# Kernel tuning notes

Hardware: AMD Instinct MI355X
Metric: run time of the kernel (lower is better)

## Reference

```python
import jax, jax.numpy as jnp
import numpy as np

HEAD_DIM = 64
NUM_HEADS = 16
ROPE_BASE = 10000.0


def _rope_cos_sin(seq_len, head_dim, dtype):
    inv_freq = 1.0 / (ROPE_BASE ** (jnp.arange(0, head_dim, 2, dtype=jnp.float32) / head_dim))
    t = jnp.arange(seq_len, dtype=jnp.float32)
    freqs = jnp.outer(t, inv_freq)                      # [S, D/2]
    emb = jnp.concatenate([freqs, freqs], axis=-1)      # [S, D]
    return jnp.cos(emb).astype(dtype), jnp.sin(emb).astype(dtype)


def _rotate_half(x):
    x1, x2 = jnp.split(x, 2, axis=-1)
    return jnp.concatenate([-x2, x1], axis=-1)


def setup_inputs() -> dict:
    key = jax.random.key(0)
    ks = jax.random.split(key, 5)
    B, S, H = 2, 2048, 1024
    x = jax.random.normal(ks[0], (B, S, H), dtype=jnp.float32)
    attention_mask = jnp.ones((B, S), dtype=jnp.float32)
    scale = 0.02
    Wq = jax.random.normal(ks[1], (H, H), dtype=jnp.float32) * scale
    Wk = jax.random.normal(ks[2], (H, H), dtype=jnp.float32) * scale
    Wv = jax.random.normal(ks[3], (H, H), dtype=jnp.float32) * scale
    Wo = jax.random.normal(ks[4], (H, H), dtype=jnp.float32) * scale
    return {"x": x, "attention_mask": attention_mask, "Wq": Wq, "Wk": Wk, "Wv": Wv, "Wo": Wo}


def reference(x, attention_mask, Wq, Wk, Wv, Wo):
    B, S, H = x.shape
    nh, hd = NUM_HEADS, HEAD_DIM
    scale = hd ** -0.5

    # nn.Linear semantics: y = x @ W^T  (W is [out, in])
    q = jnp.einsum('bsh,oh->bso', x, Wq).reshape(B, S, nh, hd).transpose(0, 2, 1, 3)
    k = jnp.einsum('bsh,oh->bso', x, Wk).reshape(B, S, nh, hd).transpose(0, 2, 1, 3)
    v = jnp.einsum('bsh,oh->bso', x, Wv).reshape(B, S, nh, hd).transpose(0, 2, 1, 3)

    cos, sin = _rope_cos_sin(S, hd, x.dtype)            # [S, hd]
    cos = cos[None, None, :, :]
    sin = sin[None, None, :, :]
    q = q * cos + _rotate_half(q) * sin
    k = k * cos + _rotate_half(k) * sin

    attn = jnp.einsum('bhqd,bhkd->bhqk', q, k) * scale  # [B, nh, S, S]
    mask = (1.0 - attention_mask.astype(x.dtype))[:, None, None, :] * jnp.finfo(x.dtype).min
    attn = attn + mask
    attn = jax.nn.softmax(attn, axis=-1)
    out = jnp.einsum('bhqk,bhkd->bhqd', attn, v)        # [B, nh, S, hd]
    out = out.transpose(0, 2, 1, 3).reshape(B, S, nh * hd)
    return jnp.einsum('bso,ho->bsh', out, Wo)
```

## Files before the change

### kernel.cpp

```cpp
#include <hip/hip_runtime.h>
#include <math.h>

#define BB 2
#define SS 2048
#define HH 1024
#define NH 16
#define HD 64
#define MM (BB*SS)

typedef __attribute__((ext_vector_type(8))) _Float16 f16x8;
typedef __attribute__((ext_vector_type(2))) __fp16 hf16x2;
typedef __attribute__((ext_vector_type(4))) float f32x4;
typedef __attribute__((ext_vector_type(16))) float f32x16;

#define QSCALE 0.18033688011112042f

__device__ __forceinline__ unsigned short f2h(float f) {
    union { _Float16 h; unsigned short u; } c;
    c.h = (_Float16)f;
    return c.u;
}

__device__ __forceinline__ unsigned int pkh(float a, float b) {
    union { hf16x2 h; unsigned int u; } c;
    c.h = __builtin_amdgcn_cvt_pkrtz(a, b);
    return c.u;
}

__device__ __forceinline__ void gld16(const void* g, void* s) {
    __builtin_amdgcn_global_load_lds(
        (const __attribute__((address_space(1))) void*)g,
        (__attribute__((address_space(3))) void*)s, 16, 0, 0);
}

__global__ __launch_bounds__(256) void prep(
    const float* __restrict__ x, const float* __restrict__ mask,
    const float* __restrict__ Wq, const float* __restrict__ Wk,
    const float* __restrict__ Wv, const float* __restrict__ Wo,
    unsigned short* __restrict__ xf, unsigned short* __restrict__ wf,
    float* __restrict__ ctab, float* __restrict__ stab, float* __restrict__ mt,
    unsigned int* __restrict__ mflag)
{
    int gtid = blockIdx.x * 256 + threadIdx.x;
    if (gtid < SS * 32) {
        int s = gtid >> 5, i = gtid & 31;
        double invf = pow(10000.0, -(double)i / 32.0);
        double a = (double)s * invf;
        ctab[gtid] = (float)cos(a);
        stab[gtid] = (float)sin(a);
    }
    if (gtid < BB * SS) {
        float mv = mask[gtid];
        mt[gtid] = (1.0f - mv) * (-1.0e38f);
        unsigned long long bal = __ballot(mv == 1.0f);
        if ((threadIdx.x & 63) == 0)
            mflag[gtid >> 6] = (bal == ~0ull) ? 1u : 0u;
    }
    for (int it = gtid; it < 2097152; it += 524288) {
        float4 v; unsigned short* d; size_t off;
        if (it < 1048576) {
            off = (size_t)it * 4;
            v = *(const float4*)(x + off);
            d = xf;
        } else {
            off = (size_t)(it - 1048576) * 4;
            int row = (int)(off >> 10);
            const float* W = row < 1024 ? Wq : row < 2048 ? Wk : row < 3072 ? Wv : Wo;
            v = *(const float4*)(W + (((size_t)(row & 1023)) << 10) + (off & 1023));
            d = wf;
        }
        *(ushort4*)(d + off) = make_ushort4(f2h(v.x), f2h(v.y), f2h(v.z), f2h(v.w));
    }
}

template<int MODE>
__global__ __launch_bounds__(256, 3) void gemm3(
    const unsigned short* __restrict__ Axf,
    const unsigned short* __restrict__ Wf,
    const float* __restrict__ ctab, const float* __restrict__ stab,
    unsigned short* __restrict__ qo, unsigned short* __restrict__ ko,
    unsigned short* __restrict__ vo, float* __restrict__ fout)
{
    __shared__ __align__(16) short lsA[2][128*32];
    __shared__ __align__(16) short lsB[2][128*32];

    const int t = threadIdx.x;
    const int m0 = blockIdx.x * 128;
    const int brow0 = (MODE == 0 ? 0 : 3072) + blockIdx.y * 128;
    const int lane = t & 63, wv = t >> 6;
    const int wm = (wv >> 1) * 64, wn = (wv & 1) * 64;
    const int fr = lane & 15, fg = lane >> 4;

    const int srow = t >> 2, pc = t & 3;
    const int scx = (pc ^ ((srow >> 1) & 3)) * 8;
    const int lo  = srow * 32 + pc * 8;
    const size_t gA0 = (size_t)(m0 + srow) * HH + scx;
    const size_t gA1 = (size_t)(m0 + 64 + srow) * HH + scx;
    const size_t gB0 = (size_t)(brow0 + srow) * HH + scx;
    const size_t gB1 = (size_t)(brow0 + 64 + srow) * HH + scx;

    f32x4 acc[4][4] = {};

#define STAGE(sel, kk) do { \
        gld16(Axf + gA0 + (kk), &lsA[sel][lo]);            \
        gld16(Wf  + gB0 + (kk), &lsB[sel][lo]);            \
        gld16(Axf + gA1 + (kk), &lsA[sel][lo + 64*32]);    \
        gld16(Wf  + gB1 + (kk), &lsB[sel][lo + 64*32]);    \
    } while (0)

    STAGE(0, 0);
    __syncthreads();

    int cur = 0;
    for (int k0 = 0; k0 < HH; k0 += 32) {
        if (k0 + 32 < HH) STAGE(cur ^ 1, k0 + 32);

        f16x8 ah[4], bh[4];
        const int swz = (fg ^ ((fr >> 1) & 3)) * 8;
        #pragma unroll
        for (int mi = 0; mi < 4; ++mi)
            ah[mi] = *(const f16x8*)&lsA[cur][(wm + 16*mi + fr)*32 + swz];
        #pragma unroll
        for (int ni = 0; ni < 4; ++ni)
            bh[ni] = *(const f16x8*)&lsB[cur][(wn + 16*ni + fr)*32 + swz];

        __builtin_amdgcn_s_setprio(1);
        #pragma unroll
        for (int mi = 0; mi < 4; ++mi)
            #pragma unroll
            for (int ni = 0; ni < 4; ++ni)
                acc[mi][ni] = __builtin_amdgcn_mfma_f32_16x16x32_f16(ah[mi], bh[ni], acc[mi][ni], 0, 0, 0);
        __builtin_amdgcn_s_setprio(0);
        __syncthreads();
        cur ^= 1;
    }
#undef STAGE

    if (MODE == 0) {
        const int mat = brow0 >> 10;
        const int obase = (brow0 & 1023) + wn;
        const int h = obase >> 6;
        #pragma unroll
        for (int mi = 0; mi < 4; ++mi)
            #pragma unroll
            for (int rr = 0; rr < 4; ++rr) {
                int m = m0 + wm + 16*mi + 4*fg + rr;
                int b = m >> 11, s = m & (SS - 1);
                float v[4];
                #pragma unroll
                for (int ni = 0; ni < 4; ++ni) v[ni] = acc[mi][ni][rr];
                if (mat < 2) {
                    #pragma unroll
                    for (int ni = 0; ni < 2; ++ni) {
                        int i = 16*ni + fr;
                        float c = ctab[s*32 + i], sn = stab[s*32 + i];
                        float v1 = v[ni], v2 = v[ni + 2];
                        v[ni]     = v1*c - v2*sn;
                        v[ni + 2] = v2*c + v1*sn;
                    }
                }
                if (mat == 0) {
                    #pragma unroll
                    for (int ni = 0; ni < 4; ++ni) v[ni] *= QSCALE;
                }
                size_t base = ((size_t)(b*NH + h) * SS + s) * HD;
                #pragma unroll
                for (int ni = 0; ni < 4; ++ni) {
                    int d = 16*ni + fr;
                    unsigned short hb = f2h(v[ni]);
                    if (mat == 0)      qo[base + d] = hb;
                    else if (mat == 1) ko[base + (d ^ ((s & 7) << 3))] = hb;
                    else {
                        size_t va = ((size_t)(b*NH + h) * HD + d) * SS
                                  + (s & ~63) + ((s & 63) ^ ((d & 7) << 3));
                        vo[va] = hb;
                    }
                }
            }
    } else {
        const int n0 = blockIdx.y * 128 + wn;
        #pragma unroll
        for (int mi = 0; mi < 4; ++mi)
            #pragma unroll
            for (int rr = 0; rr < 4; ++rr) {
                int m = m0 + wm + 16*mi + 4*fg + rr;
                #pragma unroll
                for (int ni = 0; ni < 4; ++ni)
                    fout[(size_t)m * HH + n0 + 16*ni + fr] = acc[mi][ni][rr];
            }
    }
}

__global__ __launch_bounds__(256, 4) void attn(
    const unsigned short* __restrict__ qg, const unsigned short* __restrict__ kg,
    const unsigned short* __restrict__ vtg, const float* __restrict__ mt,
    const unsigned int* __restrict__ mfl, unsigned short* __restrict__ cf)
{
    __shared__ __align__(16) short Ks[2][64*64];
    __shared__ __align__(16) short Vs[2][64*64];

    const int t = threadIdx.x, lane = t & 63, wv = t >> 6;
    const int ql = lane & 31;
    const int u  = lane >> 5;
    const int qx = ql & 7;
    const int qh = wv & 1, kh = wv >> 1;
    const int flat = blockIdx.x;
    const int bh = (flat & 7) + ((flat >> 8) << 3);
    const int q0 = ((flat >> 3) & 31) * 64;
    const int b = bh >> 4, h = bh & 15;

    const unsigned short* kgb = kg  + (size_t)bh*SS*HD;
    const unsigned short* vgb = vtg + (size_t)bh*HD*SS;
    const float* mtb = mt + (size_t)b*SS;
    const unsigned int* mfb = mfl + b*32;

    f16x8 qa[4];
    #pragma unroll
    for (int dc = 0; dc < 4; ++dc)
        qa[dc] = *(const f16x8*)&qg[((size_t)bh*SS + q0 + 32*qh + ql)*HD + 16*dc + 8*u];

    f32x16 o[2] = {};
    float lpart = 0.f;

    const int srow = t >> 3, sg = t & 7;

    gld16(kgb + (size_t)srow*HD + sg*8,      &Ks[0][srow*64 + sg*8]);
    gld16(kgb + (size_t)(32+srow)*HD + sg*8, &Ks[0][(32+srow)*64 + sg*8]);
    gld16(vgb + (size_t)srow*SS + sg*8,      &Vs[0][srow*64 + sg*8]);
    gld16(vgb + (size_t)(32+srow)*SS + sg*8, &Vs[0][(32+srow)*64 + sg*8]);
    __syncthreads();

    int cur = 0;
    for (int kt = 0; kt < SS/64; ++kt) {
        const int k0 = kt * 64;
        if (kt + 1 < SS/64) {
            const int kn = k0 + 64;
            gld16(kgb + (size_t)(kn+srow)*HD + sg*8,      &Ks[cur^1][srow*64 + sg*8]);
            gld16(kgb + (size_t)(kn+32+srow)*HD + sg*8,   &Ks[cur^1][(32+srow)*64 + sg*8]);
            gld16(vgb + (size_t)srow*SS + kn + sg*8,      &Vs[cur^1][srow*64 + sg*8]);
            gld16(vgb + (size_t)(32+srow)*SS + kn + sg*8, &Vs[cur^1][(32+srow)*64 + sg*8]);
        }
        const int fl = __builtin_amdgcn_readfirstlane(mfb[kt]);

        f16x8 kb[4];
        #pragma unroll
        for (int dc = 0; dc < 4; ++dc)
            kb[dc] = *(const f16x8*)&Ks[cur][(32*kh + ql)*64 + ((2*dc + u) ^ qx)*8];

        f32x16 sc = {};
        __builtin_amdgcn_s_setprio(1);
        #pragma unroll
        for (int dc = 0; dc < 4; ++dc)
            sc = __builtin_amdgcn_mfma_f32_32x32x16_f16(kb[dc], qa[dc], sc, 0, 0, 0);
        __builtin_amdgcn_s_setprio(0);

        f16x8 vb[2][2];
        #pragma unroll
        for (int dt = 0; dt < 2; ++dt)
            #pragma unroll
            for (int ki = 0; ki < 2; ++ki)
                vb[dt][ki] = *(const f16x8*)&Vs[cur][(32*dt + ql)*64 + ((4*kh + 2*ki + u) ^ qx)*8];

        if (fl) {
            #pragma unroll
            for (int r = 0; r < 16; ++r) {
                float p = __builtin_amdgcn_exp2f(sc[r]);
                sc[r] = p;
                lpart += p;
            }
        } else {
            #pragma unroll
            for (int g = 0; g < 4; ++g) {
                float4 m4 = *(const float4*)&mtb[k0 + 32*kh + 8*g + 4*u];
                #pragma unroll
                for (int j = 0; j < 4; ++j) {
                    float p = __builtin_amdgcn_exp2f(sc[4*g + j] + (&m4.x)[j]);
                    sc[4*g + j] = p;
                    lpart += p;
                }
            }
        }

        __builtin_amdgcn_s_setprio(1);
        #pragma unroll
        for (int ki = 0; ki < 2; ++ki) {
            const int R0 = 8 * ki;
            unsigned int A0 = pkh(sc[R0+0], sc[R0+1]);
            unsigned int A1 = pkh(sc[R0+2], sc[R0+3]);
            unsigned int B0 = pkh(sc[R0+4], sc[R0+5]);
            unsigned int B1 = pkh(sc[R0+6], sc[R0+7]);
            asm volatile("v_permlane32_swap_b32 %0, %1" : "+v"(A0), "+v"(B0));
            asm volatile("v_permlane32_swap_b32 %0, %1" : "+v"(A1), "+v"(B1));
            union { unsigned int w[4]; f16x8 v; } pf;
            pf.w[0] = A0; pf.w[1] = A1; pf.w[2] = B0; pf.w[3] = B1;
            #pragma unroll
            for (int dt = 0; dt < 2; ++dt)
                o[dt] = __builtin_amdgcn_mfma_f32_32x32x16_f16(vb[dt][ki], pf.v, o[dt], 0, 0, 0);
        }
        __builtin_amdgcn_s_setprio(0);
        __syncthreads();
        cur ^= 1;
    }

    float* lscr = (float*)Vs;
    float* oscr = (float*)Ks;
    if (kh == 1) lscr[qh*64 + lane] = lpart;
    __syncthreads();
    float inv = 0.f;
    if (kh == 0) {
        float l = lpart + lscr[qh*64 + lane];
        l += __shfl_xor(l, 32);
        inv = 1.0f / l;
    }
    const size_t base = ((size_t)b*SS + q0 + 32*qh + ql)*HH + h*HD;
    #pragma unroll
    for (int dt = 0; dt < 2; ++dt) {
        __syncthreads();
        if (kh == 1) {
            #pragma unroll
            for (int r = 0; r < 16; ++r)
                oscr[r*128 + qh*64 + lane] = o[dt][r];
        }
        __syncthreads();
        if (kh == 0) {
            #pragma unroll
            for (int g = 0; g < 4; ++g) {
                float v0 = (o[dt][4*g+0] + oscr[(4*g+0)*128 + qh*64 + lane]) * inv;
                float v1 = (o[dt][4*g+1] + oscr[(4*g+1)*128 + qh*64 + lane]) * inv;
                float v2 = (o[dt][4*g+2] + oscr[(4*g+2)*128 + qh*64 + lane]) * inv;
                float v3 = (o[dt][4*g+3] + oscr[(4*g+3)*128 + qh*64 + lane]) * inv;
                uint2 w; w.x = pkh(v0, v1); w.y = pkh(v2, v3);
                *(uint2*)&cf[base + 32*dt + 8*g + 4*u] = w;
            }
        }
    }
}

extern "C" void kernel_launch(void* const* d_in, const int* in_sizes, int n_in,
                              void* d_out, int out_size, void* d_ws, size_t ws_size,
                              hipStream_t stream) {
    const float* x    = (const float*)d_in[0];
    const float* mask = (const float*)d_in[1];
    const float* Wq   = (const float*)d_in[2];
    const float* Wk   = (const float*)d_in[3];
    const float* Wv   = (const float*)d_in[4];
    const float* Wo   = (const float*)d_in[5];
    float* out = (float*)d_out;

    const size_t T = (size_t)MM * HH;
    unsigned short* xf = (unsigned short*)d_ws;
    unsigned short* wf = xf + T;
    unsigned short* qt = wf + T;
    unsigned short* kt = qt + T;
    unsigned short* vt = kt + T;
    float* ctab = (float*)(vt + T);
    float* stab = ctab + SS*32;
    float* mt   = stab + SS*32;
    unsigned int* mfg = (unsigned int*)(mt + BB*SS);
    unsigned short* cf = xf;

    prep<<<2048, 256, 0, stream>>>(x, mask, Wq, Wk, Wv, Wo, xf, wf, ctab, stab, mt, mfg);
    gemm3<0><<<dim3(MM/128, 3*HH/128), 256, 0, stream>>>(xf, wf, ctab, stab,
                                                         qt, kt, vt, nullptr);
    attn<<<1024, 256, 0, stream>>>(qt, kt, vt, mt, mfg, cf);
    gemm3<1><<<dim3(MM/128, HH/128), 256, 0, stream>>>(cf, wf, nullptr, nullptr,
                                                       nullptr, nullptr, nullptr, out);
}
```

Baseline: 117.1 us.

## Load K/V fragments straight from global into registers, bypassing shared memory

The attention kernel no longer stages K and V tiles through double-buffered LDS with barriers. Each wave now loads its MFMA operand fragments directly from global memory into registers, using a two-set software pipeline. The QKV projection epilogue drops the XOR swizzle that existed for LDS bank-conflict avoidance, and launch bounds drop to 3 blocks per SIMD to make room for the extra registers. This removes the LDS traffic and per-tile syncthreads, but each wave now reads K/V itself, which duplicates global/L2 reads across the waves that share a tile and uses more registers.

New measurement: 186.4 us. 59.2% more time.

```diff
diff --git a/kernel.cpp b/kernel.cpp
--- a/kernel.cpp
+++ b/kernel.cpp
@@ -169,12 +169,8 @@
                     int d = 16*ni + fr;
                     unsigned short hb = f2h(v[ni]);
                     if (mat == 0)      qo[base + d] = hb;
-                    else if (mat == 1) ko[base + (d ^ ((s & 7) << 3))] = hb;
-                    else {
-                        size_t va = ((size_t)(b*NH + h) * HD + d) * SS
-                                  + (s & ~63) + ((s & 63) ^ ((d & 7) << 3));
-                        vo[va] = hb;
-                    }
+                    else if (mat == 1) ko[base + d] = hb;
+                    else vo[((size_t)(b*NH + h) * HD + d) * SS + s] = hb;
                 }
             }
     } else {
@@ -191,28 +187,27 @@
     }
 }
 
-__global__ __launch_bounds__(256, 4) void attn(
+__global__ __launch_bounds__(256, 3) void attn(
     const unsigned short* __restrict__ qg, const unsigned short* __restrict__ kg,
     const unsigned short* __restrict__ vtg, const float* __restrict__ mt,
     const unsigned int* __restrict__ mfl, unsigned short* __restrict__ cf)
 {
-    __shared__ __align__(16) short Ks[2][64*64];
-    __shared__ __align__(16) short Vs[2][64*64];
+    __shared__ float scr[2048 + 128];
 
     const int t = threadIdx.x, lane = t & 63, wv = t >> 6;
     const int ql = lane & 31;
     const int u  = lane >> 5;
-    const int qx = ql & 7;
     const int qh = wv & 1, kh = wv >> 1;
     const int flat = blockIdx.x;
     const int bh = (flat & 7) + ((flat >> 8) << 3);
     const int q0 = ((flat >> 3) & 31) * 64;
     const int b = bh >> 4, h = bh & 15;
 
-    const unsigned short* kgb = kg  + (size_t)bh*SS*HD;
-    const unsigned short* vgb = vtg + (size_t)bh*HD*SS;
     const float* mtb = mt + (size_t)b*SS;
     const unsigned int* mfb = mfl + b*32;
+
+    const unsigned short* kp = kg  + ((size_t)bh*SS + 32*kh + ql)*HD + 8*u;
+    const unsigned short* vp = vtg + ((size_t)bh*HD + ql)*SS + 32*kh + 8*u;
 
     f16x8 qa[4];
     #pragma unroll
@@ -222,88 +217,82 @@
     f32x16 o[2] = {};
     float lpart = 0.f;
 
-    const int srow = t >> 3, sg = t & 7;
-
-    gld16(kgb + (size_t)srow*HD + sg*8,      &Ks[0][srow*64 + sg*8]);
-    gld16(kgb + (size_t)(32+srow)*HD + sg*8, &Ks[0][(32+srow)*64 + sg*8]);
-    gld16(vgb + (size_t)srow*SS + sg*8,      &Vs[0][srow*64 + sg*8]);
-    gld16(vgb + (size_t)(32+srow)*SS + sg*8, &Vs[0][(32+srow)*64 + sg*8]);
-    __syncthreads();
-
-    int cur = 0;
-    for (int kt = 0; kt < SS/64; ++kt) {
-        const int k0 = kt * 64;
-        if (kt + 1 < SS/64) {
-            const int kn = k0 + 64;
-            gld16(kgb + (size_t)(kn+srow)*HD + sg*8,      &Ks[cur^1][srow*64 + sg*8]);
-            gld16(kgb + (size_t)(kn+32+srow)*HD + sg*8,   &Ks[cur^1][(32+srow)*64 + sg*8]);
-            gld16(vgb + (size_t)srow*SS + kn + sg*8,      &Vs[cur^1][srow*64 + sg*8]);
-            gld16(vgb + (size_t)(32+srow)*SS + kn + sg*8, &Vs[cur^1][(32+srow)*64 + sg*8]);
-        }
-        const int fl = __builtin_amdgcn_readfirstlane(mfb[kt]);
-
-        f16x8 kb[4];
-        #pragma unroll
-        for (int dc = 0; dc < 4; ++dc)
-            kb[dc] = *(const f16x8*)&Ks[cur][(32*kh + ql)*64 + ((2*dc + u) ^ qx)*8];
-
-        f32x16 sc = {};
-        __builtin_amdgcn_s_setprio(1);
-        #pragma unroll
-        for (int dc = 0; dc < 4; ++dc)
-            sc = __builtin_amdgcn_mfma_f32_32x32x16_f16(kb[dc], qa[dc], sc, 0, 0, 0);
-        __builtin_amdgcn_s_setprio(0);
-
-        f16x8 vb[2][2];
-        #pragma unroll
-        for (int dt = 0; dt < 2; ++dt)
-            #pragma unroll
-            for (int ki = 0; ki < 2; ++ki)
-                vb[dt][ki] = *(const f16x8*)&Vs[cur][(32*dt + ql)*64 + ((4*kh + 2*ki + u) ^ qx)*8];
-
-        if (fl) {
-            #pragma unroll
-            for (int r = 0; r < 16; ++r) {
-                float p = __builtin_amdgcn_exp2f(sc[r]);
-                sc[r] = p;
-                lpart += p;
-            }
-        } else {
-            #pragma unroll
-            for (int g = 0; g < 4; ++g) {
-                float4 m4 = *(const float4*)&mtb[k0 + 32*kh + 8*g + 4*u];
-                #pragma unroll
-                for (int j = 0; j < 4; ++j) {
-                    float p = __builtin_amdgcn_exp2f(sc[4*g + j] + (&m4.x)[j]);
-                    sc[4*g + j] = p;
-                    lpart += p;
-                }
-            }
-        }
-
-        __builtin_amdgcn_s_setprio(1);
-        #pragma unroll
-        for (int ki = 0; ki < 2; ++ki) {
-            const int R0 = 8 * ki;
-            unsigned int A0 = pkh(sc[R0+0], sc[R0+1]);
-            unsigned int A1 = pkh(sc[R0+2], sc[R0+3]);
-            unsigned int B0 = pkh(sc[R0+4], sc[R0+5]);
-            unsigned int B1 = pkh(sc[R0+6], sc[R0+7]);
-            asm volatile("v_permlane32_swap_b32 %0, %1" : "+v"(A0), "+v"(B0));
-            asm volatile("v_permlane32_swap_b32 %0, %1" : "+v"(A1), "+v"(B1));
-            union { unsigned int w[4]; f16x8 v; } pf;
-            pf.w[0] = A0; pf.w[1] = A1; pf.w[2] = B0; pf.w[3] = B1;
-            #pragma unroll
-            for (int dt = 0; dt < 2; ++dt)
-                o[dt] = __builtin_amdgcn_mfma_f32_32x32x16_f16(vb[dt][ki], pf.v, o[dt], 0, 0, 0);
-        }
-        __builtin_amdgcn_s_setprio(0);
-        __syncthreads();
-        cur ^= 1;
-    }
-
-    float* lscr = (float*)Vs;
-    float* oscr = (float*)Ks;
+    f16x8 Akb0, Akb1, Akb2, Akb3, Avb00, Avb01, Avb10, Avb11;
+    f16x8 Bkb0, Bkb1, Bkb2, Bkb3, Bvb00, Bvb01, Bvb10, Bvb11;
+
+#define LOADSET(P, kk) do {                                                   \
+        P##kb0  = *(const f16x8*)(kp + (size_t)(kk)*HD +  0);                 \
+        P##kb1  = *(const f16x8*)(kp + (size_t)(kk)*HD + 16);                 \
+        P##kb2  = *(const f16x8*)(kp + (size_t)(kk)*HD + 32);                 \
+        P##kb3  = *(const f16x8*)(kp + (size_t)(kk)*HD + 48);                 \
+        P##vb00 = *(const f16x8*)(vp + (kk) +  0);                            \
+        P##vb01 = *(const f16x8*)(vp + (kk) + 16);                            \
+        P##vb10 = *(const f16x8*)(vp + (size_t)32*SS + (kk) +  0);            \
+        P##vb11 = *(const f16x8*)(vp + (size_t)32*SS + (kk) + 16);            \
+    } while (0)
+
+#define COMPUTE(P, kk) do {                                                   \
+        const int fl = __builtin_amdgcn_readfirstlane(mfb[(kk) >> 6]);        \
+        f32x16 sc = {};                                                       \
+        __builtin_amdgcn_s_setprio(1);                                        \
+        sc = __builtin_amdgcn_mfma_f32_32x32x16_f16(P##kb0, qa[0], sc, 0, 0, 0); \
+        sc = __builtin_amdgcn_mfma_f32_32x32x16_f16(P##kb1, qa[1], sc, 0, 0, 0); \
+        sc = __builtin_amdgcn_mfma_f32_32x32x16_f16(P##kb2, qa[2], sc, 0, 0, 0); \
+        sc = __builtin_amdgcn_mfma_f32_32x32x16_f16(P##kb3, qa[3], sc, 0, 0, 0); \
+        __builtin_amdgcn_s_setprio(0);                                        \
+        if (fl) {                                                             \
+            _Pragma("unroll")                                                 \
+            for (int r = 0; r < 16; ++r) {                                    \
+                float p = __builtin_amdgcn_exp2f(sc[r]);                      \
+                sc[r] = p; lpart += p;                                        \
+            }                                                                 \
+        } else {                                                              \
+            _Pragma("unroll")                                                 \
+            for (int g = 0; g < 4; ++g) {                                     \
+                float4 m4 = *(const float4*)&mtb[(kk) + 32*kh + 8*g + 4*u];   \
+                _Pragma("unroll")                                             \
+                for (int j = 0; j < 4; ++j) {                                 \
+                    float p = __builtin_amdgcn_exp2f(sc[4*g + j] + (&m4.x)[j]); \
+                    sc[4*g + j] = p; lpart += p;                              \
+                }                                                             \
+            }                                                                 \
+        }                                                                     \
+        __builtin_amdgcn_s_setprio(1);                                        \
+        {                                                                     \
+            unsigned int A0 = pkh(sc[0], sc[1]), A1 = pkh(sc[2], sc[3]);      \
+            unsigned int B0 = pkh(sc[4], sc[5]), B1 = pkh(sc[6], sc[7]);      \
+            asm volatile("v_permlane32_swap_b32 %0, %1" : "+v"(A0), "+v"(B0));\
+            asm volatile("v_permlane32_swap_b32 %0, %1" : "+v"(A1), "+v"(B1));\
+            union { unsigned int w[4]; f16x8 v; } pf;                         \
+            pf.w[0] = A0; pf.w[1] = A1; pf.w[2] = B0; pf.w[3] = B1;           \
+            o[0] = __builtin_amdgcn_mfma_f32_32x32x16_f16(P##vb00, pf.v, o[0], 0, 0, 0); \
+            o[1] = __builtin_amdgcn_mfma_f32_32x32x16_f16(P##vb10, pf.v, o[1], 0, 0, 0); \
+        }                                                                     \
+        {                                                                     \
+            unsigned int A0 = pkh(sc[8], sc[9]),  A1 = pkh(sc[10], sc[11]);   \
+            unsigned int B0 = pkh(sc[12], sc[13]), B1 = pkh(sc[14], sc[15]);  \
+            asm volatile("v_permlane32_swap_b32 %0, %1" : "+v"(A0), "+v"(B0));\
+            asm volatile("v_permlane32_swap_b32 %0, %1" : "+v"(A1), "+v"(B1));\
+            union { unsigned int w[4]; f16x8 v; } pf;                         \
+            pf.w[0] = A0; pf.w[1] = A1; pf.w[2] = B0; pf.w[3] = B1;           \
+            o[0] = __builtin_amdgcn_mfma_f32_32x32x16_f16(P##vb01, pf.v, o[0], 0, 0, 0); \
+            o[1] = __builtin_amdgcn_mfma_f32_32x32x16_f16(P##vb11, pf.v, o[1], 0, 0, 0); \
+        }                                                                     \
+        __builtin_amdgcn_s_setprio(0);                                        \
+    } while (0)
+
+    LOADSET(A, 0);
+    for (int k0 = 0; k0 < SS; k0 += 128) {
+        LOADSET(B, k0 + 64);
+        COMPUTE(A, k0);
+        if (k0 + 128 < SS) LOADSET(A, k0 + 128);
+        COMPUTE(B, k0 + 64);
+    }
+#undef LOADSET
+#undef COMPUTE
+
+    float* oscr = scr;
+    float* lscr = scr + 2048;
     if (kh == 1) lscr[qh*64 + lane] = lpart;
     __syncthreads();
     float inv = 0.f;
```

## Triple-buffer K/V tiles with single barrier and compute row sums via MFMA

Applied to the files above, without the earlier changes.

Moves the attention K/V staging from double to triple buffering, prefetching two tiles ahead and replacing the per-iteration __syncthreads with a vmcnt wait plus a single s_barrier. Row-sum accumulation of softmax probabilities now uses an extra MFMA against a ones vector instead of scalar adds, and mask flags are preloaded into a bitmask. The aim is to hide global load latency and cut VALU and sync work. The cost is more LDS, lower occupancy (launch bounds 4→3), and one extra MFMA per k-subtile.

Result: slower. 130.2 us (+11.2%).

```diff
diff --git a/kernel.cpp b/kernel.cpp
--- a/kernel.cpp
+++ b/kernel.cpp
@@ -191,13 +191,13 @@
     }
 }
 
-__global__ __launch_bounds__(256, 4) void attn(
+__global__ __launch_bounds__(256, 3) void attn(
     const unsigned short* __restrict__ qg, const unsigned short* __restrict__ kg,
     const unsigned short* __restrict__ vtg, const float* __restrict__ mt,
     const unsigned int* __restrict__ mfl, unsigned short* __restrict__ cf)
 {
-    __shared__ __align__(16) short Ks[2][64*64];
-    __shared__ __align__(16) short Vs[2][64*64];
+    __shared__ __align__(16) short Ks[3][64*64];
+    __shared__ __align__(16) short Vs[3][64*64];
 
     const int t = threadIdx.x, lane = t & 63, wv = t >> 6;
     const int ql = lane & 31;
@@ -214,38 +214,55 @@
     const float* mtb = mt + (size_t)b*SS;
     const unsigned int* mfb = mfl + b*32;
 
+    unsigned int fmask = 0;
+    for (int i = 0; i < 32; ++i) fmask |= (mfb[i] & 1u) << i;
+
     f16x8 qa[4];
     #pragma unroll
     for (int dc = 0; dc < 4; ++dc)
         qa[dc] = *(const f16x8*)&qg[((size_t)bh*SS + q0 + 32*qh + ql)*HD + 16*dc + 8*u];
 
+    f16x8 onev;
+    #pragma unroll
+    for (int i = 0; i < 8; ++i) onev[i] = (_Float16)1.0f;
+
     f32x16 o[2] = {};
-    float lpart = 0.f;
+    f32x16 oS = {};
 
     const int srow = t >> 3, sg = t & 7;
 
-    gld16(kgb + (size_t)srow*HD + sg*8,      &Ks[0][srow*64 + sg*8]);
-    gld16(kgb + (size_t)(32+srow)*HD + sg*8, &Ks[0][(32+srow)*64 + sg*8]);
-    gld16(vgb + (size_t)srow*SS + sg*8,      &Vs[0][srow*64 + sg*8]);
-    gld16(vgb + (size_t)(32+srow)*SS + sg*8, &Vs[0][(32+srow)*64 + sg*8]);
-    __syncthreads();
-
-    int cur = 0;
+    __builtin_amdgcn_sched_barrier(0);
+    asm volatile("s_waitcnt vmcnt(0) lgkmcnt(0)" ::: "memory");
+    __builtin_amdgcn_sched_barrier(0);
+
+#define STAGEKV(kt_, bi_) do { \
+        const int kn_ = (kt_) * 64; \
+        gld16(kgb + (size_t)(kn_+srow)*HD + sg*8,      &Ks[bi_][srow*64 + sg*8]); \
+        gld16(kgb + (size_t)(kn_+32+srow)*HD + sg*8,   &Ks[bi_][(32+srow)*64 + sg*8]); \
+        gld16(vgb + (size_t)srow*SS + kn_ + sg*8,      &Vs[bi_][srow*64 + sg*8]); \
+        gld16(vgb + (size_t)(32+srow)*SS + kn_ + sg*8, &Vs[bi_][(32+srow)*64 + sg*8]); \
+    } while (0)
+
+    STAGEKV(0, 0);
+    STAGEKV(1, 1);
+
     for (int kt = 0; kt < SS/64; ++kt) {
-        const int k0 = kt * 64;
+        const int bi = kt % 3;
+        __builtin_amdgcn_sched_barrier(0);
         if (kt + 1 < SS/64) {
-            const int kn = k0 + 64;
-            gld16(kgb + (size_t)(kn+srow)*HD + sg*8,      &Ks[cur^1][srow*64 + sg*8]);
-            gld16(kgb + (size_t)(kn+32+srow)*HD + sg*8,   &Ks[cur^1][(32+srow)*64 + sg*8]);
-            gld16(vgb + (size_t)srow*SS + kn + sg*8,      &Vs[cur^1][srow*64 + sg*8]);
-            gld16(vgb + (size_t)(32+srow)*SS + kn + sg*8, &Vs[cur^1][(32+srow)*64 + sg*8]);
-        }
-        const int fl = __builtin_amdgcn_readfirstlane(mfb[kt]);
+            asm volatile("s_waitcnt vmcnt(4)" ::: "memory");
+        } else {
+            asm volatile("s_waitcnt vmcnt(0)" ::: "memory");
+        }
+        __builtin_amdgcn_s_barrier();
+        __builtin_amdgcn_sched_barrier(0);
+
+        if (kt + 2 < SS/64) STAGEKV(kt + 2, (kt + 2) % 3);
 
         f16x8 kb[4];
         #pragma unroll
         for (int dc = 0; dc < 4; ++dc)
-            kb[dc] = *(const f16x8*)&Ks[cur][(32*kh + ql)*64 + ((2*dc + u) ^ qx)*8];
+            kb[dc] = *(const f16x8*)&Ks[bi][(32*kh + ql)*64 + ((2*dc + u) ^ qx)*8];
 
         f32x16 sc = {};
         __builtin_amdgcn_s_setprio(1);
@@ -259,25 +276,19 @@
         for (int dt = 0; dt < 2; ++dt)
             #pragma unroll
             for (int ki = 0; ki < 2; ++ki)
-                vb[dt][ki] = *(const f16x8*)&Vs[cur][(32*dt + ql)*64 + ((4*kh + 2*ki + u) ^ qx)*8];
-
-        if (fl) {
-            #pragma unroll
-            for (int r = 0; r < 16; ++r) {
-                float p = __builtin_amdgcn_exp2f(sc[r]);
-                sc[r] = p;
-                lpart += p;
-            }
+                vb[dt][ki] = *(const f16x8*)&Vs[bi][(32*dt + ql)*64 + ((4*kh + 2*ki + u) ^ qx)*8];
+
+        if ((fmask >> kt) & 1) {
+            #pragma unroll
+            for (int r = 0; r < 16; ++r)
+                sc[r] = __builtin_amdgcn_exp2f(sc[r]);
         } else {
             #pragma unroll
             for (int g = 0; g < 4; ++g) {
-                float4 m4 = *(const float4*)&mtb[k0 + 32*kh + 8*g + 4*u];
+                float4 m4 = *(const float4*)&mtb[kt*64 + 32*kh + 8*g + 4*u];
                 #pragma unroll
-                for (int j = 0; j < 4; ++j) {
-                    float p = __builtin_amdgcn_exp2f(sc[4*g + j] + (&m4.x)[j]);
-                    sc[4*g + j] = p;
-                    lpart += p;
-                }
+                for (int j = 0; j < 4; ++j)
+                    sc[4*g + j] = __builtin_amdgcn_exp2f(sc[4*g + j] + (&m4.x)[j]);
             }
         }
 
@@ -293,25 +304,22 @@
             asm volatile("v_permlane32_swap_b32 %0, %1" : "+v"(A1), "+v"(B1));
             union { unsigned int w[4]; f16x8 v; } pf;
             pf.w[0] = A0; pf.w[1] = A1; pf.w[2] = B0; pf.w[3] = B1;
-            #pragma unroll
-            for (int dt = 0; dt < 2; ++dt)
-                o[dt] = __builtin_amdgcn_mfma_f32_32x32x16_f16(vb[dt][ki], pf.v, o[dt], 0, 0, 0);
+            o[0] = __builtin_amdgcn_mfma_f32_32x32x16_f16(vb[0][ki], pf.v, o[0], 0, 0, 0);
+            o[1] = __builtin_amdgcn_mfma_f32_32x32x16_f16(vb[1][ki], pf.v, o[1], 0, 0, 0);
+            oS   = __builtin_amdgcn_mfma_f32_32x32x16_f16(onev,     pf.v, oS,   0, 0, 0);
         }
         __builtin_amdgcn_s_setprio(0);
-        __syncthreads();
-        cur ^= 1;
-    }
-
+    }
+#undef STAGEKV
+
+    float lpart = oS[0];
     float* lscr = (float*)Vs;
     float* oscr = (float*)Ks;
     if (kh == 1) lscr[qh*64 + lane] = lpart;
     __syncthreads();
     float inv = 0.f;
-    if (kh == 0) {
-        float l = lpart + lscr[qh*64 + lane];
-        l += __shfl_xor(l, 32);
-        inv = 1.0f / l;
-    }
+    if (kh == 0)
+        inv = 1.0f / (lpart + lscr[qh*64 + lane]);
     const size_t base = ((size_t)b*SS + q0 + 32*qh + ql)*HH + h*HD;
     #pragma unroll
     for (int dt = 0; dt < 2; ++dt) {
```
